# Optimization experiments

Measured on AMD Instinct MI355X. Metric: run time of the kernel, lower is better.

The kernel has to match this reference:

```python
import jax, jax.numpy as jnp
import numpy as np

H = 4  # num_heads
EPS = 1e-12


def _mhsa(x, wq, bq, wk, bk, wv, bv, wo, bo):
    # x: [N, A, B, E]; attention over axis B within each (N, A)
    N, A, B, E = x.shape
    d = E // H
    q = (x @ wq + bq).reshape(N, A, B, H, d)
    k = (x @ wk + bk).reshape(N, A, B, H, d)
    v = (x @ wv + bv).reshape(N, A, B, H, d)
    s = jnp.einsum('naqhd,nakhd->nahqk', q, k) / (d ** 0.5)
    a = jax.nn.softmax(s, axis=-1)
    o = jnp.einsum('nahqk,nakhd->naqhd', a, v).reshape(N, A, B, E)
    return o @ wo + bo


def setup_inputs() -> dict:
    key = jax.random.key(0)
    ks = jax.random.split(key, 32)
    N, C, T, V, E, NC = 1024, 3, 30, 14, 64, 7
    g = lambda k, shape, s=0.05: (jax.random.normal(k, shape, dtype=jnp.float32) * s)
    inp = {
        'x_joint': jax.random.normal(ks[0], (N, C, T, V), dtype=jnp.float32),
        'x_vel': jax.random.normal(ks[1], (N, C, T, V), dtype=jnp.float32),
        'je_w': g(ks[2], (C, E)), 'je_b': g(ks[3], (E,)),
        've_w': g(ks[4], (C, E)), 've_b': g(ks[5], (E,)),
        'joint_emb': g(ks[6], (V, E)), 'frame_emb': g(ks[7], (T, E)),
        'proj_w': g(ks[8], (3 * E, E)), 'proj_b': g(ks[9], (E,)),
        'gcn_w1': g(ks[10], (E, E)), 'gcn_b1': g(ks[11], (E,)),
        'gcn_w2': g(ks[12], (E, E)), 'gcn_b2': g(ks[13], (E,)),
        'sa_wq': g(ks[14], (E, E)), 'sa_bq': g(ks[15], (E,)),
        'sa_wk': g(ks[16], (E, E)), 'sa_bk': g(ks[17], (E,)),
        'sa_wv': g(ks[18], (E, E)), 'sa_bv': g(ks[19], (E,)),
        'sa_wo': g(ks[20], (E, E)), 'sa_bo': g(ks[21], (E,)),
        'ta_wq': g(ks[22], (E, E)), 'ta_bq': g(ks[23], (E,)),
        'ta_wk': g(ks[24], (E, E)), 'ta_bk': g(ks[25], (E,)),
        'ta_wv': g(ks[26], (E, E)), 'ta_bv': g(ks[27], (E,)),
        'ta_wo': g(ks[28], (E, E)), 'ta_bo': g(ks[29], (E,)),
        'fc_w': g(ks[30], (E, NC)), 'fc_b': g(ks[31], (NC,)),
    }
    return inp


def reference(x_joint, x_vel, je_w, je_b, ve_w, ve_b, joint_emb, frame_emb,
              proj_w, proj_b, gcn_w1, gcn_b1, gcn_w2, gcn_b2,
              sa_wq, sa_bq, sa_wk, sa_bk, sa_wv, sa_bv, sa_wo, sa_bo,
              ta_wq, ta_bq, ta_wk, ta_bk, ta_wv, ta_bv, ta_wo, ta_bo,
              fc_w, fc_b):
    N, C, T, V = x_joint.shape
    E = je_w.shape[1]
    # 1x1 convs (pointwise over channels) -> [N, T, V, E]
    f = (jnp.einsum('nctv,ce->ntve', x_joint, je_w) + je_b
         + jnp.einsum('nctv,ce->ntve', x_vel, ve_w) + ve_b)
    jE = jnp.broadcast_to(joint_emb[None, None, :, :], (N, T, V, E))
    fE = jnp.broadcast_to(frame_emb[None, :, None, :], (N, T, V, E))
    feat = jnp.concatenate([f, jE, fE], axis=-1) @ proj_w + proj_b  # [N,T,V,E]
    # attention adjacency over joints per frame
    nf = feat / jnp.maximum(jnp.linalg.norm(feat, axis=-1, keepdims=True), EPS)
    adj = jax.nn.softmax(nf @ jnp.swapaxes(nf, -1, -2), axis=-1)  # [N,T,V,V]
    feat = adj @ feat
    feat = jax.nn.relu(feat @ gcn_w1 + gcn_b1) @ gcn_w2 + gcn_b2
    # spatial attention (over V) with residual
    feat = _mhsa(feat, sa_wq, sa_bq, sa_wk, sa_bk, sa_wv, sa_bv, sa_wo, sa_bo) + feat
    # temporal attention (over T) with residual
    ft = jnp.swapaxes(feat, 1, 2)  # [N,V,T,E]
    ft = _mhsa(ft, ta_wq, ta_bq, ta_wk, ta_bk, ta_wv, ta_bv, ta_wo, ta_bo) + ft
    feat = jnp.swapaxes(ft, 1, 2)  # [N,T,V,E]
    pooled = jnp.max(feat, axis=(1, 2))  # adaptive max pool over (T,V)
    return pooled @ fc_w + fc_b
```

## Files before the change

kernel.cpp:

```cpp
#include <hip/hip_runtime.h>
#include <math.h>

#define C_ 3
#define T_ 30
#define V_ 14
#define E_ 64
#define H_ 4
#define D_ 16
#define NC_ 7

#define SW_ 72
#define SV_ 20

typedef unsigned short u16;
typedef __attribute__((ext_vector_type(8))) short bf16x8;
typedef __attribute__((ext_vector_type(4))) short bf16x4;
typedef __attribute__((ext_vector_type(4))) float f32x4;
typedef __attribute__((ext_vector_type(16))) float f32x16;

__device__ __forceinline__ float4 f4_load(const float* p) {
    return *reinterpret_cast<const float4*>(p);
}
__device__ __forceinline__ float4 f4_add(float4 a, float4 b) {
    return make_float4(a.x + b.x, a.y + b.y, a.z + b.z, a.w + b.w);
}
__device__ __forceinline__ float4 f4_fma(float a, float4 b, float4 c) {
    c.x = fmaf(a, b.x, c.x); c.y = fmaf(a, b.y, c.y);
    c.z = fmaf(a, b.z, c.z); c.w = fmaf(a, b.w, c.w); return c;
}
__device__ __forceinline__ u16 f2bf(float x) {
    union { __bf16 b; u16 u; } cv;
    cv.b = (__bf16)x;
    return cv.u;
}
__device__ __forceinline__ uint2 pack4bf(float4 f) {
    return make_uint2((unsigned)f2bf(f.x) | ((unsigned)f2bf(f.y) << 16),
                      (unsigned)f2bf(f.z) | ((unsigned)f2bf(f.w) << 16));
}
__device__ __forceinline__ f32x16 f16z() {
    return (f32x16){0.f,0.f,0.f,0.f, 0.f,0.f,0.f,0.f, 0.f,0.f,0.f,0.f, 0.f,0.f,0.f,0.f};
}
__device__ __forceinline__ bf16x8 ld_frag8(const u16* p) {
    bf16x4 lo = *(const bf16x4*)p;
    bf16x4 hi = *(const bf16x4*)(p + 4);
    return __builtin_shufflevector(lo, hi, 0, 1, 2, 3, 4, 5, 6, 7);
}

__global__ void k_setup(const float* __restrict__ je_w, const float* __restrict__ je_b,
                        const float* __restrict__ ve_w, const float* __restrict__ ve_b,
                        const float* __restrict__ joint_emb, const float* __restrict__ frame_emb,
                        const float* __restrict__ proj_w, const float* __restrict__ proj_b,
                        const float* __restrict__ twq, const float* __restrict__ twk,
                        const float* __restrict__ twv, const float* __restrict__ two,
                        const float* __restrict__ sw1, const float* __restrict__ sw2,
                        const float* __restrict__ swq, const float* __restrict__ swk,
                        const float* __restrict__ swv, const float* __restrict__ swo,
                        float* __restrict__ tab) {
    int e = threadIdx.x;
    int b = blockIdx.x;
    if (b >= 1 && b <= 10) {
        int m = b - 1;
        const float* Ws[10] = {twq, twk, twv, two, sw1, sw2, swq, swk, swv, swo};
        const float* W = Ws[m];
        u16* wt = (u16*)(tab + 3200);
        for (int i = 0; i < E_; ++i)
            wt[m * 4096 + e * 64 + i] = f2bf(W[i * E_ + e]);
        return;
    }
    if (b >= 11) {
        float bias = proj_b[e];
        for (int i = 0; i < E_; ++i) bias += (je_b[i] + ve_b[i]) * proj_w[i * E_ + e];
        int t0 = (b - 11) * 10;
        for (int t = t0; t < t0 + 10; ++t) {
            float s = bias;
            for (int i = 0; i < E_; ++i) s += frame_emb[t * E_ + i] * proj_w[(128 + i) * E_ + e];
            tab[1280 + t * E_ + e] = s;
        }
        return;
    }
    for (int c = 0; c < C_; ++c) {
        float aj = 0.f, av = 0.f;
        for (int i = 0; i < E_; ++i) {
            float p0 = proj_w[i * E_ + e];
            aj += je_w[c * E_ + i] * p0;
            av += ve_w[c * E_ + i] * p0;
        }
        tab[c * E_ + e] = aj;
        tab[192 + c * E_ + e] = av;
    }
    for (int v = 0; v < V_; ++v) {
        float s = 0.f;
        for (int i = 0; i < E_; ++i) s += joint_emb[v * E_ + i] * proj_w[(64 + i) * E_ + e];
        tab[384 + v * E_ + e] = s;
    }
}

__global__ __launch_bounds__(64) void k_spatial(
    const float* __restrict__ xj, const float* __restrict__ xv,
    const float* __restrict__ tab, const u16* __restrict__ wt16,
    const float* __restrict__ b1, const float* __restrict__ b2,
    const float* __restrict__ bq, const float* __restrict__ bk,
    const float* __restrict__ bv, const float* __restrict__ bo,
    float* __restrict__ feat1) {
    int ntb = blockIdx.x;
    int n = ntb / T_;
    int t = ntb % T_;
    int tid = threadIdx.x;
    int dcol = tid & 15;
    int kgrp = tid >> 4;
    int trow4 = kgrp * 4;
    int e4 = dcol << 2;
    int r4 = kgrp;
    int l32 = tid & 31;
    int half = tid >> 5;

    const u16* w1T = wt16 + 4 * 4096;
    const u16* w2T = wt16 + 5 * 4096;
    const u16* wqT = wt16 + 6 * 4096;
    const u16* wkT = wt16 + 7 * 4096;
    const u16* wvT = wt16 + 8 * 4096;
    const u16* woT = wt16 + 9 * 4096;

    __shared__ __align__(16) u16 sm[6272];
    u16* feat16 = sm;
    u16* g1out  = sm;
    u16* ao16   = sm;
    u16* fT16   = sm + 1152;
    u16* qkvin  = sm + 1152;
    float* adjraw = (float*)(sm + 2432);
    u16* g1in   = sm + 2432;
    u16* qs16   = sm + 2432;
    u16* ps16   = sm + 2432;
    float* scb  = (float*)sm;
    u16* adjs16 = sm + 3712;
    u16* ks16   = sm + 3712;
    u16* vsT16  = sm + 4992;
    float* xs   = (float*)(sm + 4992);

    for (int o = tid; o < 2 * C_ * V_; o += 64) {
        int s = o / (C_ * V_);
        int rem = o % (C_ * V_);
        int c = rem / V_, v = rem % V_;
        const float* src = s ? xv : xj;
        xs[(s * C_ + c) * V_ + v] = src[((size_t)(n * C_ + c) * T_ + t) * V_ + v];
    }
    __syncthreads();

    {
        float4 F = f4_load(tab + 1280 + t * E_ + e4);
        float4 AJ[C_], AV[C_];
#pragma unroll
        for (int c = 0; c < C_; ++c) {
            AJ[c] = f4_load(tab + c * E_ + e4);
            AV[c] = f4_load(tab + 192 + c * E_ + e4);
        }
#pragma unroll
        for (int j = 0; j < 4; ++j) {
            int q = r4 + 4 * j;
            if (q < V_) {
                float4 s = f4_add(F, f4_load(tab + 384 + q * E_ + e4));
#pragma unroll
                for (int c = 0; c < C_; ++c) {
                    s = f4_fma(xs[(0 * C_ + c) * V_ + q], AJ[c], s);
                    s = f4_fma(xs[(1 * C_ + c) * V_ + q], AV[c], s);
                }
                *(uint2*)&feat16[q * SW_ + e4] = pack4bf(s);
                fT16[(e4 + 0) * SV_ + q] = f2bf(s.x);
                fT16[(e4 + 1) * SV_ + q] = f2bf(s.y);
                fT16[(e4 + 2) * SV_ + q] = f2bf(s.z);
                fT16[(e4 + 3) * SV_ + q] = f2bf(s.w);
            }
        }
        fT16[tid * SV_ + 14] = 0;
        fT16[tid * SV_ + 15] = 0;
    }
    __syncthreads();

    {
        bf16x8 f0 = *(bf16x8*)&feat16[dcol * SW_ + kgrp * 8];
        bf16x8 f1 = *(bf16x8*)&feat16[dcol * SW_ + 32 + kgrp * 8];
        f32x4 d = (f32x4){0.f, 0.f, 0.f, 0.f};
        d = __builtin_amdgcn_mfma_f32_16x16x32_bf16(f0, f0, d, 0, 0, 0);
        d = __builtin_amdgcn_mfma_f32_16x16x32_bf16(f1, f1, d, 0, 0, 0);
#pragma unroll
        for (int r = 0; r < 4; ++r) {
            int row = trow4 + r;
            if (row < V_) adjraw[row * 18 + dcol] = d[r];
        }
    }
    __syncthreads();

    if (tid < 4 * V_) {
        int row = tid >> 2, g = tid & 3;
        float iq = 1.0f / fmaxf(sqrtf(adjraw[row * 18 + row]), 1e-12f);
        float c[4];
        float m = -1e30f;
#pragma unroll
        for (int j = 0; j < 4; ++j) {
            int k = g * 4 + j;
            if (k < V_) {
                float ik = 1.0f / fmaxf(sqrtf(adjraw[k * 18 + k]), 1e-12f);
                c[j] = adjraw[row * 18 + k] * iq * ik;
            } else {
                c[j] = -1e30f;
            }
            m = fmaxf(m, c[j]);
        }
        m = fmaxf(m, __shfl_xor(m, 1));
        m = fmaxf(m, __shfl_xor(m, 2));
        float su = 0.f;
#pragma unroll
        for (int j = 0; j < 4; ++j) { c[j] = __expf(c[j] - m); su += c[j]; }
        su += __shfl_xor(su, 1);
        su += __shfl_xor(su, 2);
        float iv = 1.f / su;
#pragma unroll
        for (int j = 0; j < 4; ++j) {
            int k = g * 4 + j;
            if (k < V_) adjs16[row * SV_ + k] = f2bf(c[j] * iv);
        }
        if (g == 3) {
            adjs16[row * SV_ + 14] = 0;
            adjs16[row * SV_ + 15] = 0;
        }
    }
    __syncthreads();

    {
        bf16x8 aA = ld_frag8(&adjs16[l32 * SV_ + half * 8]);
#pragma unroll
        for (int nt = 0; nt < 2; ++nt) {
            bf16x8 bB = ld_frag8(&fT16[(nt * 32 + l32) * SV_ + half * 8]);
            f32x16 g = f16z();
            g = __builtin_amdgcn_mfma_f32_32x32x16_bf16(aA, bB, g, 0, 0, 0);
#pragma unroll
            for (int reg = 0; reg < 16; ++reg) {
                int row = (reg & 3) + 8 * (reg >> 2) + 4 * half;
                if (row < V_) g1in[row * SW_ + nt * 32 + l32] = f2bf(g[reg]);
            }
        }
    }
    __syncthreads();

    {
        bf16x8 a0 = *(bf16x8*)&g1in[dcol * SW_ + kgrp * 8];
        bf16x8 a1 = *(bf16x8*)&g1in[dcol * SW_ + 32 + kgrp * 8];
#pragma unroll
        for (int nt = 0; nt < 4; ++nt) {
            int col = nt * 16 + dcol;
            float bb = b1[col];
            f32x4 cc = (f32x4){bb, bb, bb, bb};
            cc = __builtin_amdgcn_mfma_f32_16x16x32_bf16(a0, *(const bf16x8*)&w1T[col * 64 + kgrp * 8], cc, 0, 0, 0);
            cc = __builtin_amdgcn_mfma_f32_16x16x32_bf16(a1, *(const bf16x8*)&w1T[col * 64 + 32 + kgrp * 8], cc, 0, 0, 0);
#pragma unroll
            for (int r = 0; r < 4; ++r) {
                int row = trow4 + r;
                if (row < V_) g1out[row * SW_ + col] = f2bf(fmaxf(cc[r], 0.f));
            }
        }
    }
    __syncthreads();

    f32x4 fresr[4];
    {
        bf16x8 a0 = *(bf16x8*)&g1out[dcol * SW_ + kgrp * 8];
        bf16x8 a1 = *(bf16x8*)&g1out[dcol * SW_ + 32 + kgrp * 8];
#pragma unroll
        for (int nt = 0; nt < 4; ++nt) {
            int col = nt * 16 + dcol;
            float bb = b2[col];
            f32x4 cc = (f32x4){bb, bb, bb, bb};
            cc = __builtin_amdgcn_mfma_f32_16x16x32_bf16(a0, *(const bf16x8*)&w2T[col * 64 + kgrp * 8], cc, 0, 0, 0);
            cc = __builtin_amdgcn_mfma_f32_16x16x32_bf16(a1, *(const bf16x8*)&w2T[col * 64 + 32 + kgrp * 8], cc, 0, 0, 0);
            fresr[nt] = cc;
#pragma unroll
            for (int r = 0; r < 4; ++r) {
                int row = trow4 + r;
                if (row < V_) qkvin[row * SW_ + col] = f2bf(cc[r]);
            }
        }
    }
    __syncthreads();

    {
        bf16x8 a0 = *(bf16x8*)&qkvin[dcol * SW_ + kgrp * 8];
        bf16x8 a1 = *(bf16x8*)&qkvin[dcol * SW_ + 32 + kgrp * 8];
#pragma unroll
        for (int nt = 0; nt < 4; ++nt) {
            int col = nt * 16 + dcol;
            float bqs = bq[col], bks = bk[col], bvs = bv[col];
            f32x4 cq = (f32x4){bqs, bqs, bqs, bqs};
            f32x4 ck = (f32x4){bks, bks, bks, bks};
            f32x4 cv = (f32x4){bvs, bvs, bvs, bvs};
            cq = __builtin_amdgcn_mfma_f32_16x16x32_bf16(a0, *(const bf16x8*)&wqT[col * 64 + kgrp * 8], cq, 0, 0, 0);
            cq = __builtin_amdgcn_mfma_f32_16x16x32_bf16(a1, *(const bf16x8*)&wqT[col * 64 + 32 + kgrp * 8], cq, 0, 0, 0);
            ck = __builtin_amdgcn_mfma_f32_16x16x32_bf16(a0, *(const bf16x8*)&wkT[col * 64 + kgrp * 8], ck, 0, 0, 0);
            ck = __builtin_amdgcn_mfma_f32_16x16x32_bf16(a1, *(const bf16x8*)&wkT[col * 64 + 32 + kgrp * 8], ck, 0, 0, 0);
            cv = __builtin_amdgcn_mfma_f32_16x16x32_bf16(a0, *(const bf16x8*)&wvT[col * 64 + kgrp * 8], cv, 0, 0, 0);
            cv = __builtin_amdgcn_mfma_f32_16x16x32_bf16(a1, *(const bf16x8*)&wvT[col * 64 + 32 + kgrp * 8], cv, 0, 0, 0);
            int pair = nt >> 1, hw = nt & 1;
            u16* qsb = qs16 + pair * 640;
            u16* ksb = ks16 + pair * 640;
            u16* vtb = vsT16 + pair * 640;
#pragma unroll
            for (int r = 0; r < 4; ++r) {
                int row = trow4 + r;
                qsb[(hw * 16 + row) * SV_ + dcol] = f2bf(cq[r]);
                ksb[(hw * 16 + row) * SV_ + dcol] = f2bf(ck[r]);
                vtb[(hw * 16 + dcol) * SV_ + row] = (row < V_) ? f2bf(cv[r]) : (u16)0;
            }
        }
    }
    __syncthreads();

    {
#pragma unroll
        for (int pair = 0; pair < 2; ++pair) {
            bf16x8 aq = ld_frag8(&qs16[pair * 640 + l32 * SV_ + half * 8]);
            bf16x8 bk8 = ld_frag8(&ks16[pair * 640 + l32 * SV_ + half * 8]);
            f32x16 d = f16z();
            d = __builtin_amdgcn_mfma_f32_32x32x16_bf16(aq, bk8, d, 0, 0, 0);
            int kp = l32 & 15, hp = l32 >> 4;
            if (kp < V_) {
#pragma unroll
                for (int reg = 0; reg < 16; ++reg) {
                    int row = (reg & 3) + 8 * (reg >> 2) + 4 * half;
                    if ((row >> 4) == hp && (row & 15) < V_)
                        scb[(pair * 2 + hp) * 252 + (row & 15) * 18 + kp] = d[reg];
                }
            }
        }
    }
    __syncthreads();

    if (tid < H_ * V_) {
        int h = tid / V_, q = tid % V_;
        float p[V_];
        float m = -1e30f;
#pragma unroll
        for (int k = 0; k < V_; ++k) { p[k] = scb[h * 252 + q * 18 + k]; m = fmaxf(m, p[k]); }
        float su = 0.f;
#pragma unroll
        for (int k = 0; k < V_; ++k) { p[k] = __expf((p[k] - m) * 0.25f); su += p[k]; }
        float iv = 1.f / su;
        u16* psb = ps16 + (h >> 1) * 640;
        int rowp = (h & 1) * 16 + q;
#pragma unroll
        for (int k = 0; k < V_; ++k) psb[rowp * SV_ + k] = f2bf(p[k] * iv);
        psb[rowp * SV_ + 14] = 0;
        psb[rowp * SV_ + 15] = 0;
    }
    __syncthreads();

    {
#pragma unroll
        for (int pair = 0; pair < 2; ++pair) {
            bf16x8 ap = ld_frag8(&ps16[pair * 640 + l32 * SV_ + half * 8]);
            bf16x8 bv8 = ld_frag8(&vsT16[pair * 640 + l32 * SV_ + half * 8]);
            f32x16 d = f16z();
            d = __builtin_amdgcn_mfma_f32_32x32x16_bf16(ap, bv8, d, 0, 0, 0);
            int np = l32 & 15, hp = l32 >> 4;
#pragma unroll
            for (int reg = 0; reg < 16; ++reg) {
                int row = (reg & 3) + 8 * (reg >> 2) + 4 * half;
                if ((row >> 4) == hp && (row & 15) < V_)
                    ao16[(row & 15) * SW_ + (pair * 2 + hp) * 16 + np] = f2bf(d[reg]);
            }
        }
    }
    __syncthreads();

    {
        bf16x8 a0 = *(bf16x8*)&ao16[dcol * SW_ + kgrp * 8];
        bf16x8 a1 = *(bf16x8*)&ao16[dcol * SW_ + 32 + kgrp * 8];
        float* dst = feat1 + (size_t)ntb * (V_ * E_);
#pragma unroll
        for (int nt = 0; nt < 4; ++nt) {
            int col = nt * 16 + dcol;
            float bos = bo[col];
            f32x4 cc = (f32x4){bos, bos, bos, bos};
            cc = __builtin_amdgcn_mfma_f32_16x16x32_bf16(a0, *(const bf16x8*)&woT[col * 64 + kgrp * 8], cc, 0, 0, 0);
            cc = __builtin_amdgcn_mfma_f32_16x16x32_bf16(a1, *(const bf16x8*)&woT[col * 64 + 32 + kgrp * 8], cc, 0, 0, 0);
#pragma unroll
            for (int r = 0; r < 4; ++r) {
                int row = trow4 + r;
                if (row < V_) dst[row * E_ + col] = cc[r] + fresr[nt][r];
            }
        }
    }
}

__global__ __launch_bounds__(64) void k_temporal(
    const float* __restrict__ feat1,
    const u16* __restrict__ wt16,
    const float* __restrict__ bq, const float* __restrict__ bk,
    const float* __restrict__ bv, const float* __restrict__ bo,
    float* __restrict__ tmax) {
    int nv = blockIdx.x;
    int n = nv / V_;
    int v = nv % V_;
    int tid = threadIdx.x;
    int dcol = tid & 15;
    int kgrp = tid >> 4;
    int trow4 = kgrp * 4;
    int l32 = tid & 31;
    int half = tid >> 5;

    const u16* wtq = wt16;
    const u16* wtk = wt16 + 4096;
    const u16* wtv = wt16 + 8192;
    const u16* wto = wt16 + 12288;

    __shared__ __align__(16) u16 smt[6464];
    u16*  ft16 = smt;
    float* scb = (float*)smt;
    u16*  ao16 = smt + 2304;
    u16*  qs16 = smt + 4608;
    u16*  ks16 = smt + 5248;
    u16*  ps16 = smt + 4608;
    u16*  vT16 = smt + 5888;

    const float* fsrc = feat1 + ((size_t)n * T_ * V_ + v) * E_;

    for (int o = tid; o < T_ * 16; o += 64) {
        int t = o >> 4, c4i = (o & 15) << 2;
        float4 f = f4_load(fsrc + (size_t)t * V_ * E_ + c4i);
        *(uint2*)&ft16[t * 72 + c4i] = pack4bf(f);
    }
    __syncthreads();

    bf16x8 af[2][2];
#pragma unroll
    for (int mt = 0; mt < 2; ++mt)
#pragma unroll
        for (int ks = 0; ks < 2; ++ks)
            af[mt][ks] = *(bf16x8*)&ft16[(mt * 16 + dcol) * 72 + ks * 32 + kgrp * 8];

    bool sact = (tid < 2 * T_);
    int sq = sact ? (tid >> 1) : 0;
    int kbase = (tid & 1) * 15;

    for (int h = 0; h < H_; ++h) {
        {
            float bqs = bq[h * D_ + dcol];
            float bks = bk[h * D_ + dcol];
            f32x4 qacc[2], kacc[2];
#pragma unroll
            for (int mt = 0; mt < 2; ++mt) {
                qacc[mt] = (f32x4){bqs, bqs, bqs, bqs};
                kacc[mt] = (f32x4){bks, bks, bks, bks};
            }
#pragma unroll
            for (int ks = 0; ks < 2; ++ks) {
                int boff = (h * D_ + dcol) * 64 + ks * 32 + kgrp * 8;
                bf16x8 b_q = *(const bf16x8*)&wtq[boff];
                bf16x8 b_k = *(const bf16x8*)&wtk[boff];
#pragma unroll
                for (int mt = 0; mt < 2; ++mt) {
                    qacc[mt] = __builtin_amdgcn_mfma_f32_16x16x32_bf16(af[mt][ks], b_q, qacc[mt], 0, 0, 0);
                    kacc[mt] = __builtin_amdgcn_mfma_f32_16x16x32_bf16(af[mt][ks], b_k, kacc[mt], 0, 0, 0);
                }
            }
#pragma unroll
            for (int mt = 0; mt < 2; ++mt)
#pragma unroll
                for (int r = 0; r < 4; ++r) {
                    int t = mt * 16 + trow4 + r;
                    qs16[t * SV_ + dcol] = f2bf(qacc[mt][r]);
                    ks16[t * SV_ + dcol] = f2bf(kacc[mt][r]);
                }
        }
        __syncthreads();

        {
            bf16x8 aq = ld_frag8(&qs16[l32 * SV_ + half * 8]);
            bf16x8 bk8 = ld_frag8(&ks16[l32 * SV_ + half * 8]);
            f32x16 d = f16z();
            d = __builtin_amdgcn_mfma_f32_32x32x16_bf16(aq, bk8, d, 0, 0, 0);
            if (l32 < T_) {
#pragma unroll
                for (int reg = 0; reg < 16; ++reg) {
                    int row = (reg & 3) + 8 * (reg >> 2) + 4 * half;
                    if (row < T_) scb[row * 36 + l32] = d[reg];
                }
            }
        }
        __syncthreads();

        {
            float m = -1e30f;
#pragma unroll
            for (int k = 0; k < 15; ++k) m = fmaxf(m, scb[sq * 36 + kbase + k]);
            m = fmaxf(m, __shfl_xor(m, 1));
            float ex[15];
            float su = 0.f;
#pragma unroll
            for (int k = 0; k < 15; ++k) {
                ex[k] = __expf((scb[sq * 36 + kbase + k] - m) * 0.25f);
                su += ex[k];
            }
            su += __shfl_xor(su, 1);
            float iv = 1.f / su;
            if (sact) {
#pragma unroll
                for (int k = 0; k < 15; ++k) ps16[sq * 36 + kbase + k] = f2bf(ex[k] * iv);
                if (kbase) { ps16[sq * 36 + 30] = 0; ps16[sq * 36 + 31] = 0; }
            }
        }
        {
            float bvs = bv[h * D_ + dcol];
            f32x4 vacc[2];
            vacc[0] = (f32x4){bvs, bvs, bvs, bvs};
            vacc[1] = vacc[0];
#pragma unroll
            for (int ks = 0; ks < 2; ++ks) {
                int boff = (h * D_ + dcol) * 64 + ks * 32 + kgrp * 8;
                bf16x8 b_v = *(const bf16x8*)&wtv[boff];
#pragma unroll
                for (int mt = 0; mt < 2; ++mt)
                    vacc[mt] = __builtin_amdgcn_mfma_f32_16x16x32_bf16(af[mt][ks], b_v, vacc[mt], 0, 0, 0);
            }
#pragma unroll
            for (int mt = 0; mt < 2; ++mt)
#pragma unroll
                for (int r = 0; r < 4; ++r) {
                    int t = mt * 16 + trow4 + r;
                    vT16[dcol * 36 + t] = (t < T_) ? f2bf(vacc[mt][r]) : (u16)0;
                }
        }
        __syncthreads();

        {
            bf16x8 ap0 = ld_frag8(&ps16[l32 * 36 + half * 8]);
            bf16x8 ap1 = ld_frag8(&ps16[l32 * 36 + 16 + half * 8]);
            bf16x8 bv0 = ld_frag8(&vT16[(l32 & 15) * 36 + half * 8]);
            bf16x8 bv1 = ld_frag8(&vT16[(l32 & 15) * 36 + 16 + half * 8]);
            f32x16 d = f16z();
            d = __builtin_amdgcn_mfma_f32_32x32x16_bf16(ap0, bv0, d, 0, 0, 0);
            d = __builtin_amdgcn_mfma_f32_32x32x16_bf16(ap1, bv1, d, 0, 0, 0);
            if (l32 < 16) {
#pragma unroll
                for (int reg = 0; reg < 16; ++reg) {
                    int row = (reg & 3) + 8 * (reg >> 2) + 4 * half;
                    if (row < T_) ao16[row * 72 + h * D_ + l32] = f2bf(d[reg]);
                }
            }
        }
        __syncthreads();
    }

    {
        bf16x8 oa[2][2];
#pragma unroll
        for (int mt = 0; mt < 2; ++mt)
#pragma unroll
            for (int ks = 0; ks < 2; ++ks)
                oa[mt][ks] = *(bf16x8*)&ao16[(mt * 16 + dcol) * 72 + ks * 32 + kgrp * 8];

        float mxc[4];
#pragma unroll
        for (int nt = 0; nt < 4; ++nt) {
            float bos = bo[nt * 16 + dcol];
            f32x4 oacc[2];
            oacc[0] = (f32x4){bos, bos, bos, bos};
            oacc[1] = oacc[0];
#pragma unroll
            for (int ks = 0; ks < 2; ++ks) {
                bf16x8 bb = *(const bf16x8*)&wto[(nt * 16 + dcol) * 64 + ks * 32 + kgrp * 8];
#pragma unroll
                for (int mt = 0; mt < 2; ++mt)
                    oacc[mt] = __builtin_amdgcn_mfma_f32_16x16x32_bf16(oa[mt][ks], bb, oacc[mt], 0, 0, 0);
            }
            float m = -1e30f;
#pragma unroll
            for (int mt = 0; mt < 2; ++mt)
#pragma unroll
                for (int r = 0; r < 4; ++r) {
                    int t = mt * 16 + trow4 + r;
                    if (t < T_) {
                        float rr = oacc[mt][r] +
                                   fsrc[(size_t)t * V_ * E_ + nt * 16 + dcol];
                        m = fmaxf(m, rr);
                    }
                }
            mxc[nt] = m;
        }
#pragma unroll
        for (int nt = 0; nt < 4; ++nt) {
            mxc[nt] = fmaxf(mxc[nt], __shfl_xor(mxc[nt], 16));
            mxc[nt] = fmaxf(mxc[nt], __shfl_xor(mxc[nt], 32));
        }
        if (tid < 16) {
#pragma unroll
            for (int nt = 0; nt < 4; ++nt)
                tmax[(size_t)nv * E_ + nt * 16 + tid] = mxc[nt];
        }
    }
}

__global__ void k_pool_fc(const float* __restrict__ tmax,
                          const float* __restrict__ fc_w, const float* __restrict__ fc_b,
                          float* __restrict__ out) {
    int n = blockIdx.x;
    int tid = threadIdx.x;
    __shared__ float pooled[E_];
    float m = -1e30f;
    for (int v = 0; v < V_; ++v) m = fmaxf(m, tmax[((size_t)n * V_ + v) * E_ + tid]);
    pooled[tid] = m;
    __syncthreads();
    if (tid < NC_) {
        float s = fc_b[tid];
        for (int e = 0; e < E_; ++e) s += pooled[e] * fc_w[e * NC_ + tid];
        out[n * NC_ + tid] = s;
    }
}

extern "C" void kernel_launch(void* const* d_in, const int* in_sizes, int n_in,
                              void* d_out, int out_size, void* d_ws, size_t ws_size,
                              hipStream_t stream) {
    const float* xj        = (const float*)d_in[0];
    const float* xv        = (const float*)d_in[1];
    const float* je_w      = (const float*)d_in[2];
    const float* je_b      = (const float*)d_in[3];
    const float* ve_w      = (const float*)d_in[4];
    const float* ve_b      = (const float*)d_in[5];
    const float* joint_emb = (const float*)d_in[6];
    const float* frame_emb = (const float*)d_in[7];
    const float* proj_w    = (const float*)d_in[8];
    const float* proj_b    = (const float*)d_in[9];
    const float* gcn_w1    = (const float*)d_in[10];
    const float* gcn_b1    = (const float*)d_in[11];
    const float* gcn_w2    = (const float*)d_in[12];
    const float* gcn_b2    = (const float*)d_in[13];
    const float* sa_wq     = (const float*)d_in[14];
    const float* sa_bq     = (const float*)d_in[15];
    const float* sa_wk     = (const float*)d_in[16];
    const float* sa_bk     = (const float*)d_in[17];
    const float* sa_wv     = (const float*)d_in[18];
    const float* sa_bv     = (const float*)d_in[19];
    const float* sa_wo     = (const float*)d_in[20];
    const float* sa_bo     = (const float*)d_in[21];
    const float* ta_wq     = (const float*)d_in[22];
    const float* ta_bq     = (const float*)d_in[23];
    const float* ta_wk     = (const float*)d_in[24];
    const float* ta_bk     = (const float*)d_in[25];
    const float* ta_wv     = (const float*)d_in[26];
    const float* ta_bv     = (const float*)d_in[27];
    const float* ta_wo     = (const float*)d_in[28];
    const float* ta_bo     = (const float*)d_in[29];
    const float* fc_w      = (const float*)d_in[30];
    const float* fc_b      = (const float*)d_in[31];
    float* out = (float*)d_out;

    int N = in_sizes[0] / (C_ * T_ * V_);

    float* ws    = (float*)d_ws;
    float* tab   = ws;
    u16*   wt16  = (u16*)(ws + 3200);
    float* tmax  = ws + 3200 + 20480;
    float* feat1 = tmax + (size_t)N * V_ * E_;

    k_setup<<<14, 64, 0, stream>>>(je_w, je_b, ve_w, ve_b, joint_emb, frame_emb,
                                   proj_w, proj_b,
                                   ta_wq, ta_wk, ta_wv, ta_wo,
                                   gcn_w1, gcn_w2, sa_wq, sa_wk, sa_wv, sa_wo, tab);
    k_spatial<<<N * T_, 64, 0, stream>>>(xj, xv, tab, wt16,
                                         gcn_b1, gcn_b2,
                                         sa_bq, sa_bk, sa_bv, sa_bo, feat1);
    k_temporal<<<N * V_, 64, 0, stream>>>(feat1, wt16,
                                          ta_bq, ta_bk, ta_bv, ta_bo, tmax);
    k_pool_fc<<<N, 64, 0, stream>>>(tmax, fc_w, fc_b, out);
}
```

Baseline: 362.3 us.

## Split spatial attention block work across two wavefronts per block

```diff
diff --git a/kernel.cpp b/kernel.cpp
--- a/kernel.cpp
+++ b/kernel.cpp
@@ -95,7 +95,7 @@
     }
 }
 
-__global__ __launch_bounds__(64) void k_spatial(
+__global__ __launch_bounds__(128) void k_spatial(
     const float* __restrict__ xj, const float* __restrict__ xv,
     const float* __restrict__ tab, const u16* __restrict__ wt16,
     const float* __restrict__ b1, const float* __restrict__ b2,
@@ -106,13 +106,15 @@
     int n = ntb / T_;
     int t = ntb % T_;
     int tid = threadIdx.x;
-    int dcol = tid & 15;
-    int kgrp = tid >> 4;
+    int wid = tid >> 6;
+    int lane = tid & 63;
+    int dcol = lane & 15;
+    int kgrp = (lane >> 4) & 3;
     int trow4 = kgrp * 4;
     int e4 = dcol << 2;
     int r4 = kgrp;
-    int l32 = tid & 31;
-    int half = tid >> 5;
+    int l32 = lane & 31;
+    int half = (lane >> 5) & 1;
 
     const u16* w1T = wt16 + 4 * 4096;
     const u16* w2T = wt16 + 5 * 4096;
@@ -137,7 +139,7 @@
     u16* vsT16  = sm + 4992;
     float* xs   = (float*)(sm + 4992);
 
-    for (int o = tid; o < 2 * C_ * V_; o += 64) {
+    for (int o = tid; o < 2 * C_ * V_; o += 128) {
         int s = o / (C_ * V_);
         int rem = o % (C_ * V_);
         int c = rem / V_, v = rem % V_;
@@ -155,8 +157,8 @@
             AV[c] = f4_load(tab + 192 + c * E_ + e4);
         }
 #pragma unroll
-        for (int j = 0; j < 4; ++j) {
-            int q = r4 + 4 * j;
+        for (int j = 0; j < 2; ++j) {
+            int q = r4 + 4 * (wid * 2 + j);
             if (q < V_) {
                 float4 s = f4_add(F, f4_load(tab + 384 + q * E_ + e4));
 #pragma unroll
@@ -171,12 +173,14 @@
                 fT16[(e4 + 3) * SV_ + q] = f2bf(s.w);
             }
         }
-        fT16[tid * SV_ + 14] = 0;
-        fT16[tid * SV_ + 15] = 0;
-    }
-    __syncthreads();
-
-    {
+        if (wid == 0) {
+            fT16[lane * SV_ + 14] = 0;
+            fT16[lane * SV_ + 15] = 0;
+        }
+    }
+    __syncthreads();
+
+    if (wid == 0) {
         bf16x8 f0 = *(bf16x8*)&feat16[dcol * SW_ + kgrp * 8];
         bf16x8 f1 = *(bf16x8*)&feat16[dcol * SW_ + 32 + kgrp * 8];
         f32x4 d = (f32x4){0.f, 0.f, 0.f, 0.f};
@@ -228,16 +232,14 @@
 
     {
         bf16x8 aA = ld_frag8(&adjs16[l32 * SV_ + half * 8]);
-#pragma unroll
-        for (int nt = 0; nt < 2; ++nt) {
-            bf16x8 bB = ld_frag8(&fT16[(nt * 32 + l32) * SV_ + half * 8]);
-            f32x16 g = f16z();
-            g = __builtin_amdgcn_mfma_f32_32x32x16_bf16(aA, bB, g, 0, 0, 0);
-#pragma unroll
-            for (int reg = 0; reg < 16; ++reg) {
-                int row = (reg & 3) + 8 * (reg >> 2) + 4 * half;
-                if (row < V_) g1in[row * SW_ + nt * 32 + l32] = f2bf(g[reg]);
-            }
+        int nt = wid;
+        bf16x8 bB = ld_frag8(&fT16[(nt * 32 + l32) * SV_ + half * 8]);
+        f32x16 g = f16z();
+        g = __builtin_amdgcn_mfma_f32_32x32x16_bf16(aA, bB, g, 0, 0, 0);
+#pragma unroll
+        for (int reg = 0; reg < 16; ++reg) {
+            int row = (reg & 3) + 8 * (reg >> 2) + 4 * half;
+            if (row < V_) g1in[row * SW_ + nt * 32 + l32] = f2bf(g[reg]);
         }
     }
     __syncthreads();
@@ -246,7 +248,8 @@
         bf16x8 a0 = *(bf16x8*)&g1in[dcol * SW_ + kgrp * 8];
         bf16x8 a1 = *(bf16x8*)&g1in[dcol * SW_ + 32 + kgrp * 8];
 #pragma unroll
-        for (int nt = 0; nt < 4; ++nt) {
+        for (int j = 0; j < 2; ++j) {
+            int nt = wid * 2 + j;
             int col = nt * 16 + dcol;
             float bb = b1[col];
             f32x4 cc = (f32x4){bb, bb, bb, bb};
@@ -261,18 +264,19 @@
     }
     __syncthreads();
 
-    f32x4 fresr[4];
+    f32x4 fresr[2];
     {
         bf16x8 a0 = *(bf16x8*)&g1out[dcol * SW_ + kgrp * 8];
         bf16x8 a1 = *(bf16x8*)&g1out[dcol * SW_ + 32 + kgrp * 8];
 #pragma unroll
-        for (int nt = 0; nt < 4; ++nt) {
+        for (int j = 0; j < 2; ++j) {
+            int nt = wid * 2 + j;
             int col = nt * 16 + dcol;
             float bb = b2[col];
             f32x4 cc = (f32x4){bb, bb, bb, bb};
             cc = __builtin_amdgcn_mfma_f32_16x16x32_bf16(a0, *(const bf16x8*)&w2T[col * 64 + kgrp * 8], cc, 0, 0, 0);
             cc = __builtin_amdgcn_mfma_f32_16x16x32_bf16(a1, *(const bf16x8*)&w2T[col * 64 + 32 + kgrp * 8], cc, 0, 0, 0);
-            fresr[nt] = cc;
+            fresr[j] = cc;
 #pragma unroll
             for (int r = 0; r < 4; ++r) {
                 int row = trow4 + r;
@@ -286,7 +290,8 @@
         bf16x8 a0 = *(bf16x8*)&qkvin[dcol * SW_ + kgrp * 8];
         bf16x8 a1 = *(bf16x8*)&qkvin[dcol * SW_ + 32 + kgrp * 8];
 #pragma unroll
-        for (int nt = 0; nt < 4; ++nt) {
+        for (int j = 0; j < 2; ++j) {
+            int nt = wid * 2 + j;
             int col = nt * 16 + dcol;
             float bqs = bq[col], bks = bk[col], bvs = bv[col];
             f32x4 cq = (f32x4){bqs, bqs, bqs, bqs};
@@ -298,7 +303,7 @@
             ck = __builtin_amdgcn_mfma_f32_16x16x32_bf16(a1, *(const bf16x8*)&wkT[col * 64 + 32 + kgrp * 8], ck, 0, 0, 0);
             cv = __builtin_amdgcn_mfma_f32_16x16x32_bf16(a0, *(const bf16x8*)&wvT[col * 64 + kgrp * 8], cv, 0, 0, 0);
             cv = __builtin_amdgcn_mfma_f32_16x16x32_bf16(a1, *(const bf16x8*)&wvT[col * 64 + 32 + kgrp * 8], cv, 0, 0, 0);
-            int pair = nt >> 1, hw = nt & 1;
+            int pair = wid, hw = j;
             u16* qsb = qs16 + pair * 640;
             u16* ksb = ks16 + pair * 640;
             u16* vtb = vsT16 + pair * 640;
@@ -314,27 +319,25 @@
     __syncthreads();
 
     {
-#pragma unroll
-        for (int pair = 0; pair < 2; ++pair) {
-            bf16x8 aq = ld_frag8(&qs16[pair * 640 + l32 * SV_ + half * 8]);
-            bf16x8 bk8 = ld_frag8(&ks16[pair * 640 + l32 * SV_ + half * 8]);
-            f32x16 d = f16z();
-            d = __builtin_amdgcn_mfma_f32_32x32x16_bf16(aq, bk8, d, 0, 0, 0);
-            int kp = l32 & 15, hp = l32 >> 4;
-            if (kp < V_) {
-#pragma unroll
-                for (int reg = 0; reg < 16; ++reg) {
-                    int row = (reg & 3) + 8 * (reg >> 2) + 4 * half;
-                    if ((row >> 4) == hp && (row & 15) < V_)
-                        scb[(pair * 2 + hp) * 252 + (row & 15) * 18 + kp] = d[reg];
-                }
-            }
-        }
-    }
-    __syncthreads();
-
-    if (tid < H_ * V_) {
-        int h = tid / V_, q = tid % V_;
+        int pair = wid;
+        bf16x8 aq = ld_frag8(&qs16[pair * 640 + l32 * SV_ + half * 8]);
+        bf16x8 bk8 = ld_frag8(&ks16[pair * 640 + l32 * SV_ + half * 8]);
+        f32x16 d = f16z();
+        d = __builtin_amdgcn_mfma_f32_32x32x16_bf16(aq, bk8, d, 0, 0, 0);
+        int kp = l32 & 15, hp = l32 >> 4;
+        if (kp < V_) {
+#pragma unroll
+            for (int reg = 0; reg < 16; ++reg) {
+                int row = (reg & 3) + 8 * (reg >> 2) + 4 * half;
+                if ((row >> 4) == hp && (row & 15) < V_)
+                    scb[(pair * 2 + hp) * 252 + (row & 15) * 18 + kp] = d[reg];
+            }
+        }
+    }
+    __syncthreads();
+
+    if (lane < 2 * V_) {
+        int h = wid * 2 + lane / V_, q = lane % V_;
         float p[V_];
         float m = -1e30f;
 #pragma unroll
@@ -343,7 +346,7 @@
 #pragma unroll
         for (int k = 0; k < V_; ++k) { p[k] = __expf((p[k] - m) * 0.25f); su += p[k]; }
         float iv = 1.f / su;
-        u16* psb = ps16 + (h >> 1) * 640;
+        u16* psb = ps16 + wid * 640;
         int rowp = (h & 1) * 16 + q;
 #pragma unroll
         for (int k = 0; k < V_; ++k) psb[rowp * SV_ + k] = f2bf(p[k] * iv);
@@ -353,19 +356,17 @@
     __syncthreads();
 
     {
-#pragma unroll
-        for (int pair = 0; pair < 2; ++pair) {
-            bf16x8 ap = ld_frag8(&ps16[pair * 640 + l32 * SV_ + half * 8]);
-            bf16x8 bv8 = ld_frag8(&vsT16[pair * 640 + l32 * SV_ + half * 8]);
-            f32x16 d = f16z();
-            d = __builtin_amdgcn_mfma_f32_32x32x16_bf16(ap, bv8, d, 0, 0, 0);
-            int np = l32 & 15, hp = l32 >> 4;
-#pragma unroll
-            for (int reg = 0; reg < 16; ++reg) {
-                int row = (reg & 3) + 8 * (reg >> 2) + 4 * half;
-                if ((row >> 4) == hp && (row & 15) < V_)
-                    ao16[(row & 15) * SW_ + (pair * 2 + hp) * 16 + np] = f2bf(d[reg]);
-            }
+        int pair = wid;
+        bf16x8 ap = ld_frag8(&ps16[pair * 640 + l32 * SV_ + half * 8]);
+        bf16x8 bv8 = ld_frag8(&vsT16[pair * 640 + l32 * SV_ + half * 8]);
+        f32x16 d = f16z();
+        d = __builtin_amdgcn_mfma_f32_32x32x16_bf16(ap, bv8, d, 0, 0, 0);
+        int np = l32 & 15, hp = l32 >> 4;
+#pragma unroll
+        for (int reg = 0; reg < 16; ++reg) {
+            int row = (reg & 3) + 8 * (reg >> 2) + 4 * half;
+            if ((row >> 4) == hp && (row & 15) < V_)
+                ao16[(row & 15) * SW_ + (pair * 2 + hp) * 16 + np] = f2bf(d[reg]);
         }
     }
     __syncthreads();
@@ -375,7 +376,8 @@
         bf16x8 a1 = *(bf16x8*)&ao16[dcol * SW_ + 32 + kgrp * 8];
         float* dst = feat1 + (size_t)ntb * (V_ * E_);
 #pragma unroll
-        for (int nt = 0; nt < 4; ++nt) {
+        for (int j = 0; j < 2; ++j) {
+            int nt = wid * 2 + j;
             int col = nt * 16 + dcol;
             float bos = bo[col];
             f32x4 cc = (f32x4){bos, bos, bos, bos};
@@ -384,7 +386,7 @@
 #pragma unroll
             for (int r = 0; r < 4; ++r) {
                 int row = trow4 + r;
-                if (row < V_) dst[row * E_ + col] = cc[r] + fresr[nt][r];
+                if (row < V_) dst[row * E_ + col] = cc[r] + fresr[j][r];
             }
         }
     }
@@ -664,9 +666,9 @@
                                    proj_w, proj_b,
                                    ta_wq, ta_wk, ta_wv, ta_wo,
                                    gcn_w1, gcn_w2, sa_wq, sa_wk, sa_wv, sa_wo, tab);
-    k_spatial<<<N * T_, 64, 0, stream>>>(xj, xv, tab, wt16,
-                                         gcn_b1, gcn_b2,
-                                         sa_bq, sa_bk, sa_bv, sa_bo, feat1);
+    k_spatial<<<N * T_, 128, 0, stream>>>(xj, xv, tab, wt16,
+                                          gcn_b1, gcn_b2,
+                                          sa_bq, sa_bk, sa_bv, sa_bo, feat1);
     k_temporal<<<N * V_, 64, 0, stream>>>(feat1, wt16,
                                           ta_bq, ta_bk, ta_bv, ta_bo, tmax);
     k_pool_fc<<<N, 64, 0, stream>>>(tmax, fc_w, fc_b, out);
```

After: 353.1 us. -2.5%, faster.
